# Kernel optimization log

Hardware: AMD Instinct MI355X
Metric: run time of the kernel (lower is better)

## Reference

```python
import jax, jax.numpy as jnp
import numpy as np

DIM = 256
NUM_HEADS = 4
HEAD_DIM = DIM // NUM_HEADS
SCALE = HEAD_DIM ** -0.5


def setup_inputs() -> dict:
    key = jax.random.key(0)
    ks = jax.random.split(key, 11)
    B, Nq, Nkv = 4, 2048, 2048
    inp = {
        "query_feat": jax.random.normal(ks[0], (B, Nq, DIM), dtype=jnp.float32),
        "key_value_feat": jax.random.normal(ks[1], (B, Nkv, DIM), dtype=jnp.float32),
        "reliability_kv": jax.random.uniform(ks[2], (B, Nkv), dtype=jnp.float32),
        "Wq": jax.random.normal(ks[3], (DIM, DIM), dtype=jnp.float32) * (DIM ** -0.5),
        "bq": jnp.zeros((DIM,), jnp.float32),
        "Wk": jax.random.normal(ks[4], (DIM, DIM), dtype=jnp.float32) * (DIM ** -0.5),
        "bk": jnp.zeros((DIM,), jnp.float32),
        "Wv": jax.random.normal(ks[5], (DIM, DIM), dtype=jnp.float32) * (DIM ** -0.5),
        "bv": jnp.zeros((DIM,), jnp.float32),
        "Wo": jax.random.normal(ks[6], (DIM, DIM), dtype=jnp.float32) * (DIM ** -0.5),
        "bo": jnp.zeros((DIM,), jnp.float32),
    }
    return inp


def _heads(x):
    B, N, C = x.shape
    return x.reshape(B, N, NUM_HEADS, HEAD_DIM).transpose(0, 2, 1, 3)  # [B,H,N,hd]


def reference(query_feat, key_value_feat, reliability_kv, Wq, bq, Wk, bk, Wv, bv, Wo, bo):
    B, Nq, _ = query_feat.shape
    q = _heads(query_feat @ Wq + bq)          # [B,H,Nq,hd]
    k = _heads(key_value_feat @ Wk + bk)      # [B,H,Nkv,hd]
    v = _heads(key_value_feat @ Wv + bv)
    # gate K/V by reliability (broadcast over heads and head_dim)
    rk = reliability_kv[:, None, :, None]     # [B,1,Nkv,1]
    k = k * rk
    v = v * rk
    attn = jnp.einsum("bhqd,bhkd->bhqk", q, k) * SCALE
    log_r = jnp.log(jnp.clip(reliability_kv, 1e-6))[:, None, None, :]  # [B,1,1,Nkv]
    attn = jax.nn.softmax(attn + log_r, axis=-1)  # [B,H,Nq,Nkv]
    out = jnp.einsum("bhqk,bhkd->bhqd", attn, v)
    out = out.transpose(0, 2, 1, 3).reshape(B, Nq, DIM)
    out = out @ Wo + bo
    attn_mean = attn.mean(axis=1)  # [B,Nq,Nkv]
    return out, attn_mean
```

## Files before the change

kernel.cpp:

```cpp
#include <hip/hip_runtime.h>


typedef __attribute__((ext_vector_type(8))) _Float16 half8;
typedef __attribute__((ext_vector_type(4))) _Float16 half4;
typedef __attribute__((ext_vector_type(2))) __fp16 fp16x2;
typedef __attribute__((ext_vector_type(4))) float f32x4;

#define MFMAH32(A, B, C) __builtin_amdgcn_mfma_f32_16x16x32_f16((A), (B), (C), 0, 0, 0)
#define MFMAH16(A, B, C) __builtin_amdgcn_mfma_f32_16x16x16f16((A), (B), (C), 0, 0, 0)

__device__ __forceinline__ unsigned short f2h(float f) {
    union { _Float16 h; unsigned short u; } c; c.h = (_Float16)f; return c.u;
}
__device__ __forceinline__ float h2f(unsigned short u) {
    union { unsigned short u; _Float16 h; } c; c.u = u; return (float)c.h;
}
__device__ __forceinline__ half8 ldh8(const unsigned short* p) {
    return *reinterpret_cast<const half8*>(p);
}
__device__ __forceinline__ half4 ldh4(const unsigned short* p) {
    return *reinterpret_cast<const half4*>(p);
}
__device__ __forceinline__ half4 pk4(float a, float b, float c, float d) {
    union { fp16x2 h2[2]; half4 h4; } u;
    u.h2[0] = __builtin_amdgcn_cvt_pkrtz(a, b);
    u.h2[1] = __builtin_amdgcn_cvt_pkrtz(c, d);
    return u.h4;
}
__device__ __forceinline__ void gld16(const unsigned short* g, unsigned short* l) {
    __builtin_amdgcn_global_load_lds(
        (const __attribute__((address_space(1))) unsigned int*)g,
        (__attribute__((address_space(3))) unsigned int*)l, 16, 0, 0);
}

__global__ void wsplit_kernel(const float* __restrict__ Wq, const float* __restrict__ Wk,
                              const float* __restrict__ Wv, const float* __restrict__ Wo,
                              unsigned short* __restrict__ WT) {
    int e = blockIdx.x * 256 + threadIdx.x;
    int m = e >> 16;
    int idx = e & 65535;
    int k = idx >> 8, n = idx & 255;
    const float* W = (m == 0) ? Wq : (m == 1) ? Wk : (m == 2) ? Wv : Wo;
    WT[m * 65536 + n * 256 + k] = f2h(W[idx]);
}

#define STAGE_W(dst_, src_, kt_) do {                                               \
    _Pragma("unroll")                                                               \
    for (int j_ = 0; j_ < 4; ++j_) {                                                \
        int s_ = w * 4 + j_;                                                        \
        int rowl_ = 8 * s_ + (l >> 3);                                              \
        int so_ = rowl_ * 256 + (kt_) * 64 + (((l & 7) ^ (rowl_ & 7)) << 3);        \
        gld16(&(src_)[so_], &(dst_)[s_ * 512]);                                     \
    }                                                                               \
} while (0)

#define GEMM_TILE(buf_, kt_) do {                                                   \
    _Pragma("unroll")                                                               \
    for (int ksl_ = 0; ksl_ < 2; ++ksl_) {                                          \
        _Pragma("unroll")                                                           \
        for (int n_ = 0; n_ < 16; ++n_) {                                           \
            int r_ = n_ * 16 + l15;                                                 \
            int idx_ = r_ * 64 + ((((ksl_)*4 + lg) ^ (r_ & 7)) << 3);               \
            half8 b_ = ldh8(&(buf_)[idx_]);                                         \
            acc[n_] = MFMAH32(ah[(kt_) * 2 + ksl_], b_, acc[n_]);                   \
        }                                                                           \
    }                                                                               \
} while (0)

__global__ __launch_bounds__(512, 1) void proj3_kernel(
    const float* __restrict__ query, const float* __restrict__ kv,
    const float* __restrict__ rel, const unsigned short* __restrict__ WT,
    const float* __restrict__ bq, const float* __restrict__ bk, const float* __restrict__ bv,
    unsigned short* __restrict__ Qh, unsigned short* __restrict__ Kh,
    unsigned short* __restrict__ Vtmp) {
    const int job = blockIdx.y;
    const float* X = (job == 0) ? query : kv;
    const unsigned short* wg = WT + job * 65536;
    const float* bias = (job == 0) ? bq : (job == 1) ? bk : bv;
    const float* rs = (job == 0) ? nullptr : rel;
    unsigned short* oh = (job == 0) ? Qh : (job == 1) ? Kh : Vtmp;

    __shared__ __align__(16) unsigned short wlds[2][256 * 64];

    const int w = threadIdx.x >> 6, l = threadIdx.x & 63;
    const int l15 = l & 15, lg = l >> 4;
    const int arow = blockIdx.x * 128 + w * 16 + l15;

    half8 ah[8];
#pragma unroll
    for (int ks = 0; ks < 8; ++ks) {
        const float* p = &X[arow * 256 + ks * 32 + lg * 8];
        float4 f0 = *reinterpret_cast<const float4*>(p);
        float4 f1 = *reinterpret_cast<const float4*>(p + 4);
        half8 t;
        t[0] = (_Float16)f0.x; t[1] = (_Float16)f0.y; t[2] = (_Float16)f0.z; t[3] = (_Float16)f0.w;
        t[4] = (_Float16)f1.x; t[5] = (_Float16)f1.y; t[6] = (_Float16)f1.z; t[7] = (_Float16)f1.w;
        ah[ks] = t;
    }
    f32x4 acc[16];
#pragma unroll
    for (int n = 0; n < 16; ++n) acc[n] = (f32x4){0.f, 0.f, 0.f, 0.f};

    STAGE_W(wlds[0], wg, 0);
    __syncthreads();
#pragma unroll
    for (int kt = 0; kt < 4; ++kt) {
        const int cur = kt & 1, nx = cur ^ 1;
        if (kt < 3) STAGE_W(wlds[nx], wg, kt + 1);
        GEMM_TILE(wlds[cur], kt);
        __syncthreads();
    }

    const int orow0 = blockIdx.x * 128 + w * 16 + lg * 4;
    float rsv[4];
#pragma unroll
    for (int r = 0; r < 4; ++r) rsv[r] = rs ? rs[orow0 + r] : 1.0f;
#pragma unroll
    for (int n = 0; n < 16; ++n) {
        const int col = n * 16 + l15;
        const float bn = bias[col];
#pragma unroll
        for (int r = 0; r < 4; ++r)
            oh[(orow0 + r) * 256 + col] = f2h((acc[n][r] + bn) * rsv[r]);
    }
}

__global__ void transpose_v_kernel(const unsigned short* __restrict__ Vtmp,
                                   unsigned short* __restrict__ Vt) {
    __shared__ unsigned short tile[16][264];
    const int st = blockIdx.x, b = blockIdx.y;
    const int t = threadIdx.x;
#pragma unroll
    for (int it = 0; it < 4; ++it) {
        int idx = it * 256 + t;
        int kr = idx >> 6;
        int d4 = (idx & 63) * 4;
        ushort4 v = *reinterpret_cast<const ushort4*>(
            &Vtmp[(size_t)(b * 2048 + st * 16 + kr) * 256 + d4]);
        tile[kr][d4 + 0] = v.x; tile[kr][d4 + 1] = v.y;
        tile[kr][d4 + 2] = v.z; tile[kr][d4 + 3] = v.w;
    }
    __syncthreads();
    {
        const int d = t;
        unsigned int u[8];
#pragma unroll
        for (int k2 = 0; k2 < 8; ++k2)
            u[k2] = (unsigned int)tile[k2 * 2][d] | ((unsigned int)tile[k2 * 2 + 1][d] << 16);
        uint4* dst = reinterpret_cast<uint4*>(&Vt[((size_t)(b * 128 + st) * 256 + d) * 16]);
        dst[0] = (uint4){u[0], u[1], u[2], u[3]};
        dst[1] = (uint4){u[4], u[5], u[6], u[7]};
    }
}

__global__ __launch_bounds__(512, 4) void attn_pass1(
    const unsigned short* __restrict__ Qh, const unsigned short* __restrict__ Kh,
    const unsigned short* __restrict__ Vt, const float* __restrict__ rel,
    float* __restrict__ po_a, float* __restrict__ po_b, float* __restrict__ ps) {
    const int bid = blockIdx.x;
    const int sw = (bid & 7) * 64 + (bid >> 3);
    const int b = sw >> 7;
    const int rem = sw & 127;
    const int kh = rem & 1;
    const int q0 = (rem >> 1) * 32;
    const int tid = threadIdx.x;
    const int w = tid >> 6, h = w & 3, ks = w >> 2;
    const int l = tid & 63, l15 = l & 15, lg = l >> 4;
    const float C2 = 0.18033688011112042f;

    __shared__ __align__(16) unsigned short ldsK[8][2][1024];
    __shared__ float rel_lr[2048];
    __shared__ float ssum_sh[2][4][2][16];

    {
        float4 v = reinterpret_cast<const float4*>(&rel[b * 2048])[tid];
        float* d = &rel_lr[tid * 4];
        d[0] = log2f(fmaxf(v.x, 1e-6f)); d[1] = log2f(fmaxf(v.y, 1e-6f));
        d[2] = log2f(fmaxf(v.z, 1e-6f)); d[3] = log2f(fmaxf(v.w, 1e-6f));
    }

    half8 qf[2][2];
#pragma unroll
    for (int qs = 0; qs < 2; ++qs)
#pragma unroll
        for (int kd = 0; kd < 2; ++kd)
            qf[qs][kd] = ldh8(&Qh[(b * 2048 + q0 + qs * 16 + l15) * 256 +
                                  h * 64 + kd * 32 + lg * 8]);
    __syncthreads();

    const int st0 = kh * 64 + ks * 32;

    size_t kb_[2];
    {
        const int swzK = ((l & 7) ^ ((l >> 3) & 7)) << 3;
#pragma unroll
        for (int j = 0; j < 2; ++j) {
            int kr = j * 8 + (l >> 3);
            kb_[j] = (size_t)(b * 2048 + st0 * 16 + kr) * 256 + h * 64 + swzK;
        }
    }
    size_t va_[4];
#pragma unroll
    for (int dc = 0; dc < 4; ++dc)
        va_[dc] = ((size_t)((b * 128 + st0) * 256) + h * 64 + dc * 16 + l15) * 16 + lg * 4;

    unsigned short* myK = &ldsK[w][0][0];
    const int kOff0 = l15 * 64 + ((lg ^ (l15 & 7)) << 3);
    const int kOff1 = l15 * 64 + (((4 + lg) ^ (l15 & 7)) << 3);

#define STGK(buf_, i_) do {                                                         \
    gld16(&Kh[kb_[0] + (size_t)(i_) * 4096], &myK[(buf_) * 1024]);                  \
    gld16(&Kh[kb_[1] + (size_t)(i_) * 4096], &myK[(buf_) * 1024 + 512]);            \
} while (0)
#define VLOADM(dst_, i_) do {                                                       \
    dst_[0] = ldh4(&Vt[va_[0] + (size_t)(i_) * 4096]);                              \
    dst_[1] = ldh4(&Vt[va_[1] + (size_t)(i_) * 4096]);                              \
    dst_[2] = ldh4(&Vt[va_[2] + (size_t)(i_) * 4096]);                              \
    dst_[3] = ldh4(&Vt[va_[3] + (size_t)(i_) * 4096]);                              \
} while (0)

    float ssum0 = 0.f, ssum1 = 0.f;
    f32x4 oacc0[4], oacc1[4];
#pragma unroll
    for (int dc = 0; dc < 4; ++dc) {
        oacc0[dc] = (f32x4){0.f, 0.f, 0.f, 0.f};
        oacc1[dc] = (f32x4){0.f, 0.f, 0.f, 0.f};
    }

#define COMPUTE(step_, BUF_, VF_) do {                                              \
    half8 kf0 = ldh8(&myK[(BUF_) * 1024 + kOff0]);                                  \
    half8 kf1 = ldh8(&myK[(BUF_) * 1024 + kOff1]);                                  \
    f32x4 a0 = (f32x4){0.f, 0.f, 0.f, 0.f}, a1 = a0;                                \
    a0 = MFMAH32(kf0, qf[0][0], a0); a0 = MFMAH32(kf1, qf[0][1], a0);               \
    a1 = MFMAH32(kf0, qf[1][0], a1); a1 = MFMAH32(kf1, qf[1][1], a1);               \
    float4 lr4 = *reinterpret_cast<const float4*>(                                  \
        &rel_lr[(st0 + (step_)) * 16 + lg * 4]);                                    \
    float p00 = exp2f(__builtin_fmaf(a0[0], C2, lr4.x));                            \
    float p01 = exp2f(__builtin_fmaf(a0[1], C2, lr4.y));                            \
    float p02 = exp2f(__builtin_fmaf(a0[2], C2, lr4.z));                            \
    float p03 = exp2f(__builtin_fmaf(a0[3], C2, lr4.w));                            \
    float p10 = exp2f(__builtin_fmaf(a1[0], C2, lr4.x));                            \
    float p11 = exp2f(__builtin_fmaf(a1[1], C2, lr4.y));                            \
    float p12 = exp2f(__builtin_fmaf(a1[2], C2, lr4.z));                            \
    float p13 = exp2f(__builtin_fmaf(a1[3], C2, lr4.w));                            \
    ssum0 += (p00 + p01) + (p02 + p03);                                             \
    ssum1 += (p10 + p11) + (p12 + p13);                                             \
    half4 pa0 = pk4(p00, p01, p02, p03);                                            \
    half4 pa1 = pk4(p10, p11, p12, p13);                                            \
    _Pragma("unroll")                                                               \
    for (int dc = 0; dc < 4; ++dc) {                                                \
        oacc0[dc] = MFMAH16(pa0, VF_[dc], oacc0[dc]);                               \
        oacc1[dc] = MFMAH16(pa1, VF_[dc], oacc1[dc]);                               \
    }                                                                               \
} while (0)

    half4 vfa[4], vfb[4];
    STGK(0, 0);
    VLOADM(vfa, 0);
    for (int i = 0; i < 32; i += 2) {
        STGK(1, i + 1);
        VLOADM(vfb, i + 1);
        asm volatile("s_waitcnt vmcnt(6)" ::: "memory");
        __builtin_amdgcn_sched_barrier(0);
        COMPUTE(i, 0, vfa);
        {
            const int nxt = (i + 2 < 32) ? i + 2 : 31;
            STGK(0, nxt);
            VLOADM(vfa, nxt);
        }
        asm volatile("s_waitcnt vmcnt(6)" ::: "memory");
        __builtin_amdgcn_sched_barrier(0);
        COMPUTE(i + 1, 1, vfb);
    }
    asm volatile("s_waitcnt vmcnt(0)" ::: "memory");
#undef STGK
#undef VLOADM
#undef COMPUTE

    float vr0 = ssum0, vr1 = ssum1;
    vr0 += __shfl_xor(vr0, 16); vr0 += __shfl_xor(vr0, 32);
    vr1 += __shfl_xor(vr1, 16); vr1 += __shfl_xor(vr1, 32);

    __syncthreads();
    if (l < 16) { ssum_sh[ks][h][0][l] = vr0; ssum_sh[ks][h][1][l] = vr1; }
    float* obuf = (float*)&ldsK[0][0][0];
    if (ks == 1) {
#pragma unroll
        for (int qs = 0; qs < 2; ++qs)
#pragma unroll
            for (int dc = 0; dc < 4; ++dc)
#pragma unroll
                for (int r = 0; r < 4; ++r)
                    obuf[(qs * 16 + lg * 4 + r) * 256 + h * 64 + dc * 16 + l15] =
                        (qs == 0) ? oacc0[dc][r] : oacc1[dc][r];
    }
    __syncthreads();
    if (ks == 0) {
        const int chunk = b * 2 + kh;
        float* po = (chunk < 2) ? (po_a + (size_t)chunk * 524288)
                                : (po_b + (size_t)(chunk - 2) * 524288);
#pragma unroll
        for (int qs = 0; qs < 2; ++qs)
#pragma unroll
            for (int dc = 0; dc < 4; ++dc)
#pragma unroll
                for (int r = 0; r < 4; ++r) {
                    const int d = h * 64 + dc * 16 + l15;
                    const int q = qs * 16 + lg * 4 + r;
                    const float mine = (qs == 0) ? oacc0[dc][r] : oacc1[dc][r];
                    po[(size_t)(q0 + q) * 256 + d] = mine + obuf[q * 256 + d];
                }
        if (l < 16) {
            ps[(chunk * 4 + h) * 2048 + q0 + l] =
                ssum_sh[0][h][0][l] + ssum_sh[1][h][0][l];
            ps[(chunk * 4 + h) * 2048 + q0 + 16 + l] =
                ssum_sh[0][h][1][l] + ssum_sh[1][h][1][l];
        }
    }
}

__global__ __launch_bounds__(256) void combine_kernel(
    const float* __restrict__ po_a, const float* __restrict__ po_b,
    const float* __restrict__ ps, unsigned short* __restrict__ AO,
    float* __restrict__ sinv_ws) {
    const int t = blockIdx.x * 256 + threadIdx.x;
    const int d4 = t & 63;
    const int bq = t >> 6;
    const int q = bq & 2047;
    const int b = bq >> 11;
    const int d0 = d4 * 4, h = d0 >> 6;
    const int c0 = b * 2, c1 = b * 2 + 1;
    const float* p0 = (c0 < 2) ? po_a + (size_t)c0 * 524288 : po_b + (size_t)(c0 - 2) * 524288;
    const float* p1 = (c1 < 2) ? po_a + (size_t)c1 * 524288 : po_b + (size_t)(c1 - 2) * 524288;
    float4 x = *reinterpret_cast<const float4*>(&p0[(size_t)q * 256 + d0]);
    float4 y = *reinterpret_cast<const float4*>(&p1[(size_t)q * 256 + d0]);
    float s = ps[(c0 * 4 + h) * 2048 + q] + ps[(c1 * 4 + h) * 2048 + q];
    float si = 1.0f / s;
    ushort4 o;
    o.x = f2h((x.x + y.x) * si); o.y = f2h((x.y + y.y) * si);
    o.z = f2h((x.z + y.z) * si); o.w = f2h((x.w + y.w) * si);
    *reinterpret_cast<ushort4*>(&AO[((size_t)(b * 2048 + q)) * 256 + d0]) = o;
    if (d4 == (h << 4)) sinv_ws[(b * 4 + h) * 2048 + q] = si;
}

__global__ __launch_bounds__(256, 4) void attn_mean_kernel(
    const unsigned short* __restrict__ Qh, const unsigned short* __restrict__ Kh,
    const float* __restrict__ rel, const float* __restrict__ sinv_ws,
    float* __restrict__ attn_mean) {
    const int kslice = blockIdx.x >> 7;
    const int inner = blockIdx.x & 127;
    const int sw = (inner & 7) * 16 + (inner >> 3);
    const int b = sw >> 5;
    const int q0 = (sw & 31) * 64;
    const int tid = threadIdx.x;
    const int w = tid >> 6;
    const int l = tid & 63, l15 = l & 15, lg = l >> 4;
    const int kb = b * 2048;
    const float C2 = 0.18033688011112042f;

    __shared__ __align__(16) unsigned short ldsK[2][8192];
    __shared__ float rel_lr[2048];

    {
        float4 v0 = reinterpret_cast<const float4*>(&rel[b * 2048])[tid * 2];
        float4 v1 = reinterpret_cast<const float4*>(&rel[b * 2048])[tid * 2 + 1];
        float* d = &rel_lr[tid * 8];
        d[0] = log2f(fmaxf(v0.x, 1e-6f)); d[1] = log2f(fmaxf(v0.y, 1e-6f));
        d[2] = log2f(fmaxf(v0.z, 1e-6f)); d[3] = log2f(fmaxf(v0.w, 1e-6f));
        d[4] = log2f(fmaxf(v1.x, 1e-6f)); d[5] = log2f(fmaxf(v1.y, 1e-6f));
        d[6] = log2f(fmaxf(v1.z, 1e-6f)); d[7] = log2f(fmaxf(v1.w, 1e-6f));
    }

    half8 qf[4][2];
    {
        const int qrow = b * 2048 + q0 + w * 16 + l15;
#pragma unroll
        for (int h = 0; h < 4; ++h)
#pragma unroll
            for (int kd = 0; kd < 2; ++kd)
                qf[h][kd] = ldh8(&Qh[qrow * 256 + h * 64 + kd * 32 + lg * 8]);
    }
    float lsi[4][4];
#pragma unroll
    for (int h = 0; h < 4; ++h)
#pragma unroll
        for (int r4 = 0; r4 < 4; ++r4)
            lsi[h][r4] = log2f(sinv_ws[(b * 4 + h) * 2048 + q0 + w * 16 + lg * 4 + r4]) - 2.0f;

    size_t kmb[4];
    {
#pragma unroll
        for (int j = 0; j < 4; ++j) {
            int s_ = w * 4 + j;
            int r_ = 2 * s_ + (l >> 5);
            kmb[j] = (size_t)(kb + r_) * 256 + (((l & 31) ^ (r_ & 7)) << 3);
        }
    }
#define STAGE_KM2(dst_, off_) do {                                                  \
    gld16(&Kh[kmb[0] + (off_)], &(dst_)[(w * 4 + 0) * 512]);                        \
    gld16(&Kh[kmb[1] + (off_)], &(dst_)[(w * 4 + 1) * 512]);                        \
    gld16(&Kh[kmb[2] + (off_)], &(dst_)[(w * 4 + 2) * 512]);                        \
    gld16(&Kh[kmb[3] + (off_)], &(dst_)[(w * 4 + 3) * 512]);                        \
} while (0)

    __syncthreads();

    const int kt0 = kslice * 8;
    size_t moff = (size_t)kt0 * 8192;
    STAGE_KM2(ldsK[0], moff);
    for (int ki = 0; ki < 8; ++ki) {
        const int kt = kt0 + ki;
        const int cur = ki & 1, nx = cur ^ 1;
        if (ki < 7) {
            STAGE_KM2(ldsK[nx], moff + 8192);
            moff += 8192;
            asm volatile("s_waitcnt vmcnt(4)" ::: "memory");
        } else {
            asm volatile("s_waitcnt vmcnt(0)" ::: "memory");
        }
        asm volatile("s_barrier" ::: "memory");
        __builtin_amdgcn_sched_barrier(0);
#pragma unroll
        for (int kc = 0; kc < 2; ++kc) {
            const int r = kc * 16 + l15;
            const int rx = r & 7;
            f32x4 a[4];
#pragma unroll
            for (int h = 0; h < 4; ++h) {
                half8 kf0 = ldh8(&ldsK[cur][r * 256 + (((h * 8 + lg) ^ rx) << 3)]);
                half8 kf1 = ldh8(&ldsK[cur][r * 256 + (((h * 8 + 4 + lg) ^ rx) << 3)]);
                f32x4 t = (f32x4){0.f, 0.f, 0.f, 0.f};
                t = MFMAH32(qf[h][0], kf0, t);
                t = MFMAH32(qf[h][1], kf1, t);
                a[h] = t;
            }
            const float lr = rel_lr[kt * 32 + kc * 16 + l15];
            const size_t kcol = (size_t)(kt * 32 + kc * 16 + l15);
#pragma unroll
            for (int r4 = 0; r4 < 4; ++r4) {
                float m = exp2f(__builtin_fmaf(a[0][r4], C2, lsi[0][r4]) + lr)
                        + exp2f(__builtin_fmaf(a[1][r4], C2, lsi[1][r4]) + lr)
                        + exp2f(__builtin_fmaf(a[2][r4], C2, lsi[2][r4]) + lr)
                        + exp2f(__builtin_fmaf(a[3][r4], C2, lsi[3][r4]) + lr);
                attn_mean[(size_t)(b * 2048 + q0 + w * 16 + lg * 4 + r4) * 2048 + kcol] = m;
            }
        }
        asm volatile("s_waitcnt lgkmcnt(0)\n\ts_barrier" ::: "memory");
    }
#undef STAGE_KM2
}

__global__ __launch_bounds__(512, 1) void final_kernel(
    const unsigned short* __restrict__ AO, const unsigned short* __restrict__ WoT,
    const float* __restrict__ bo, float* __restrict__ out) {
    __shared__ __align__(16) unsigned short wlds[2][256 * 64];

    const int w = threadIdx.x >> 6, l = threadIdx.x & 63;
    const int l15 = l & 15, lg = l >> 4;
    const int arow = blockIdx.x * 128 + w * 16 + l15;

    half8 ah[8];
#pragma unroll
    for (int ks = 0; ks < 8; ++ks)
        ah[ks] = ldh8(&AO[arow * 256 + ks * 32 + lg * 8]);
    f32x4 acc[16];
#pragma unroll
    for (int n = 0; n < 16; ++n) acc[n] = (f32x4){0.f, 0.f, 0.f, 0.f};

    STAGE_W(wlds[0], WoT, 0);
    __syncthreads();
#pragma unroll
    for (int kt = 0; kt < 4; ++kt) {
        const int cur = kt & 1, nx = cur ^ 1;
        if (kt < 3) STAGE_W(wlds[nx], WoT, kt + 1);
        GEMM_TILE(wlds[cur], kt);
        __syncthreads();
    }

    const int orow0 = blockIdx.x * 128 + w * 16 + lg * 4;
#pragma unroll
    for (int n = 0; n < 16; ++n) {
        const int col = n * 16 + l15;
        const float bn = bo[col];
#pragma unroll
        for (int r = 0; r < 4; ++r)
            out[(orow0 + r) * 256 + col] = acc[n][r] + bn;
    }
}

extern "C" void kernel_launch(void* const* d_in, const int* in_sizes, int n_in,
                              void* d_out, int out_size, void* d_ws, size_t ws_size,
                              hipStream_t stream) {
    const float* query = (const float*)d_in[0];
    const float* kv    = (const float*)d_in[1];
    const float* rel   = (const float*)d_in[2];
    const float* Wq    = (const float*)d_in[3];
    const float* bq    = (const float*)d_in[4];
    const float* Wk    = (const float*)d_in[5];
    const float* bk    = (const float*)d_in[6];
    const float* Wv    = (const float*)d_in[7];
    const float* bv    = (const float*)d_in[8];
    const float* Wo    = (const float*)d_in[9];
    const float* bo    = (const float*)d_in[10];

    char* ws = (char*)d_ws;
    unsigned short* WT   = (unsigned short*)(ws + 0);
    unsigned short* Qh   = (unsigned short*)(ws + 524288);
    unsigned short* Kh   = (unsigned short*)(ws + 4718592);
    unsigned short* Vtmp = (unsigned short*)(ws + 8912896);
    unsigned short* Vt   = (unsigned short*)(ws + 13107200);
    unsigned short* AO   = (unsigned short*)(ws + 17301504);
    float*          sinv = (float*)(ws + 21495808);
    float*          ps   = (float*)(ws + 21626880);
    float*          po_b = (float*)(ws + 21889024);
    float*          po_a = (float*)Vtmp;

    float* out = (float*)d_out;
    float* attn_mean = (float*)d_out + 2097152;

    wsplit_kernel<<<1024, 256, 0, stream>>>(Wq, Wk, Wv, Wo, WT);
    proj3_kernel<<<dim3(64, 3), 512, 0, stream>>>(query, kv, rel, WT,
                                                  bq, bk, bv, Qh, Kh, Vtmp);
    transpose_v_kernel<<<dim3(128, 4), 256, 0, stream>>>(Vtmp, Vt);
    attn_pass1<<<512, 512, 0, stream>>>(Qh, Kh, Vt, rel, po_a, po_b, ps);
    combine_kernel<<<2048, 256, 0, stream>>>(po_a, po_b, ps, AO, sinv);
    attn_mean_kernel<<<1024, 256, 0, stream>>>(Qh, Kh, rel, sinv, attn_mean);
    final_kernel<<<64, 512, 0, stream>>>(AO, WT + 3 * 65536, bo, out);
}
```

Baseline: 105.0 us.

## Fuse split-K combine into final GEMM and deepen attn K/V pipeline to four stages

After: 134.4 us. +28.1%, slower.

```diff
diff --git a/kernel.cpp b/kernel.cpp
--- a/kernel.cpp
+++ b/kernel.cpp
@@ -168,7 +168,7 @@
     const int l = tid & 63, l15 = l & 15, lg = l >> 4;
     const float C2 = 0.18033688011112042f;
 
-    __shared__ __align__(16) unsigned short ldsK[8][2][1024];
+    __shared__ __align__(16) unsigned short ldsK[8][4][1024];
     __shared__ float rel_lr[2048];
     __shared__ float ssum_sh[2][4][2][16];
 
@@ -208,9 +208,9 @@
     const int kOff0 = l15 * 64 + ((lg ^ (l15 & 7)) << 3);
     const int kOff1 = l15 * 64 + (((4 + lg) ^ (l15 & 7)) << 3);
 
-#define STGK(buf_, i_) do {                                                         \
-    gld16(&Kh[kb_[0] + (size_t)(i_) * 4096], &myK[(buf_) * 1024]);                  \
-    gld16(&Kh[kb_[1] + (size_t)(i_) * 4096], &myK[(buf_) * 1024 + 512]);            \
+#define STGK(slot_, i_) do {                                                        \
+    gld16(&Kh[kb_[0] + (size_t)(i_) * 4096], &myK[(slot_) * 1024]);                 \
+    gld16(&Kh[kb_[1] + (size_t)(i_) * 4096], &myK[(slot_) * 1024 + 512]);           \
 } while (0)
 #define VLOADM(dst_, i_) do {                                                       \
     dst_[0] = ldh4(&Vt[va_[0] + (size_t)(i_) * 4096]);                              \
@@ -227,9 +227,9 @@
         oacc1[dc] = (f32x4){0.f, 0.f, 0.f, 0.f};
     }
 
-#define COMPUTE(step_, BUF_, VF_) do {                                              \
-    half8 kf0 = ldh8(&myK[(BUF_) * 1024 + kOff0]);                                  \
-    half8 kf1 = ldh8(&myK[(BUF_) * 1024 + kOff1]);                                  \
+#define COMPUTE(step_, SLOT_, VF_) do {                                             \
+    half8 kf0 = ldh8(&myK[(SLOT_) * 1024 + kOff0]);                                 \
+    half8 kf1 = ldh8(&myK[(SLOT_) * 1024 + kOff1]);                                 \
     f32x4 a0 = (f32x4){0.f, 0.f, 0.f, 0.f}, a1 = a0;                                \
     a0 = MFMAH32(kf0, qf[0][0], a0); a0 = MFMAH32(kf1, qf[0][1], a0);               \
     a1 = MFMAH32(kf0, qf[1][0], a1); a1 = MFMAH32(kf1, qf[1][1], a1);               \
@@ -254,23 +254,30 @@
     }                                                                               \
 } while (0)
 
-    half4 vfa[4], vfb[4];
-    STGK(0, 0);
-    VLOADM(vfa, 0);
-    for (int i = 0; i < 32; i += 2) {
-        STGK(1, i + 1);
-        VLOADM(vfb, i + 1);
-        asm volatile("s_waitcnt vmcnt(6)" ::: "memory");
+    half4 vf0[4], vf1[4], vf2[4], vf3[4];
+    STGK(0, 0); VLOADM(vf0, 0);
+    STGK(1, 1); VLOADM(vf1, 1);
+    for (int i = 0; i < 32; i += 4) {
+        {   int nxt = (i + 2 < 32) ? i + 2 : 31;
+            STGK(2, nxt); VLOADM(vf2, nxt); }
+        asm volatile("s_waitcnt vmcnt(12)" ::: "memory");
         __builtin_amdgcn_sched_barrier(0);
-        COMPUTE(i, 0, vfa);
-        {
-            const int nxt = (i + 2 < 32) ? i + 2 : 31;
-            STGK(0, nxt);
-            VLOADM(vfa, nxt);
-        }
-        asm volatile("s_waitcnt vmcnt(6)" ::: "memory");
+        COMPUTE(i, 0, vf0);
+        {   int nxt = (i + 3 < 32) ? i + 3 : 31;
+            STGK(3, nxt); VLOADM(vf3, nxt); }
+        asm volatile("s_waitcnt vmcnt(12)" ::: "memory");
         __builtin_amdgcn_sched_barrier(0);
-        COMPUTE(i + 1, 1, vfb);
+        COMPUTE(i + 1, 1, vf1);
+        {   int nxt = (i + 4 < 32) ? i + 4 : 31;
+            STGK(0, nxt); VLOADM(vf0, nxt); }
+        asm volatile("s_waitcnt vmcnt(12)" ::: "memory");
+        __builtin_amdgcn_sched_barrier(0);
+        COMPUTE(i + 2, 2, vf2);
+        {   int nxt = (i + 5 < 32) ? i + 5 : 31;
+            STGK(1, nxt); VLOADM(vf1, nxt); }
+        asm volatile("s_waitcnt vmcnt(12)" ::: "memory");
+        __builtin_amdgcn_sched_barrier(0);
+        COMPUTE(i + 3, 3, vf3);
     }
     asm volatile("s_waitcnt vmcnt(0)" ::: "memory");
 #undef STGK
@@ -319,33 +326,9 @@
     }
 }
 
-__global__ __launch_bounds__(256) void combine_kernel(
-    const float* __restrict__ po_a, const float* __restrict__ po_b,
-    const float* __restrict__ ps, unsigned short* __restrict__ AO,
-    float* __restrict__ sinv_ws) {
-    const int t = blockIdx.x * 256 + threadIdx.x;
-    const int d4 = t & 63;
-    const int bq = t >> 6;
-    const int q = bq & 2047;
-    const int b = bq >> 11;
-    const int d0 = d4 * 4, h = d0 >> 6;
-    const int c0 = b * 2, c1 = b * 2 + 1;
-    const float* p0 = (c0 < 2) ? po_a + (size_t)c0 * 524288 : po_b + (size_t)(c0 - 2) * 524288;
-    const float* p1 = (c1 < 2) ? po_a + (size_t)c1 * 524288 : po_b + (size_t)(c1 - 2) * 524288;
-    float4 x = *reinterpret_cast<const float4*>(&p0[(size_t)q * 256 + d0]);
-    float4 y = *reinterpret_cast<const float4*>(&p1[(size_t)q * 256 + d0]);
-    float s = ps[(c0 * 4 + h) * 2048 + q] + ps[(c1 * 4 + h) * 2048 + q];
-    float si = 1.0f / s;
-    ushort4 o;
-    o.x = f2h((x.x + y.x) * si); o.y = f2h((x.y + y.y) * si);
-    o.z = f2h((x.z + y.z) * si); o.w = f2h((x.w + y.w) * si);
-    *reinterpret_cast<ushort4*>(&AO[((size_t)(b * 2048 + q)) * 256 + d0]) = o;
-    if (d4 == (h << 4)) sinv_ws[(b * 4 + h) * 2048 + q] = si;
-}
-
 __global__ __launch_bounds__(256, 4) void attn_mean_kernel(
     const unsigned short* __restrict__ Qh, const unsigned short* __restrict__ Kh,
-    const float* __restrict__ rel, const float* __restrict__ sinv_ws,
+    const float* __restrict__ rel, const float* __restrict__ ps,
     float* __restrict__ attn_mean) {
     const int kslice = blockIdx.x >> 7;
     const int inner = blockIdx.x & 127;
@@ -384,8 +367,12 @@
 #pragma unroll
     for (int h = 0; h < 4; ++h)
 #pragma unroll
-        for (int r4 = 0; r4 < 4; ++r4)
-            lsi[h][r4] = log2f(sinv_ws[(b * 4 + h) * 2048 + q0 + w * 16 + lg * 4 + r4]) - 2.0f;
+        for (int r4 = 0; r4 < 4; ++r4) {
+            const int qq = q0 + w * 16 + lg * 4 + r4;
+            float s = ps[((2 * b) * 4 + h) * 2048 + qq] +
+                      ps[((2 * b + 1) * 4 + h) * 2048 + qq];
+            lsi[h][r4] = -log2f(s) - 2.0f;
+        }
 
     size_t kmb[4];
     {
@@ -451,18 +438,40 @@
 }
 
 __global__ __launch_bounds__(512, 1) void final_kernel(
-    const unsigned short* __restrict__ AO, const unsigned short* __restrict__ WoT,
+    const float* __restrict__ po_a, const float* __restrict__ po_b,
+    const float* __restrict__ ps, const unsigned short* __restrict__ WoT,
     const float* __restrict__ bo, float* __restrict__ out) {
     __shared__ __align__(16) unsigned short wlds[2][256 * 64];
 
     const int w = threadIdx.x >> 6, l = threadIdx.x & 63;
     const int l15 = l & 15, lg = l >> 4;
     const int arow = blockIdx.x * 128 + w * 16 + l15;
+    const int bb = arow >> 11, qq = arow & 2047;
+    const int c0 = bb * 2, c1 = c0 + 1;
+    const float* p0 = (c0 < 2) ? po_a + (size_t)c0 * 524288 : po_b + (size_t)(c0 - 2) * 524288;
+    const float* p1 = (c1 < 2) ? po_a + (size_t)c1 * 524288 : po_b + (size_t)(c1 - 2) * 524288;
+
+    float si[4];
+#pragma unroll
+    for (int h = 0; h < 4; ++h)
+        si[h] = 1.0f / (ps[(c0 * 4 + h) * 2048 + qq] + ps[(c1 * 4 + h) * 2048 + qq]);
 
     half8 ah[8];
 #pragma unroll
-    for (int ks = 0; ks < 8; ++ks)
-        ah[ks] = ldh8(&AO[arow * 256 + ks * 32 + lg * 8]);
+    for (int ks = 0; ks < 8; ++ks) {
+        const int d0 = ks * 32 + lg * 8;
+        float4 x0 = *reinterpret_cast<const float4*>(&p0[(size_t)qq * 256 + d0]);
+        float4 x1 = *reinterpret_cast<const float4*>(&p0[(size_t)qq * 256 + d0 + 4]);
+        float4 y0 = *reinterpret_cast<const float4*>(&p1[(size_t)qq * 256 + d0]);
+        float4 y1 = *reinterpret_cast<const float4*>(&p1[(size_t)qq * 256 + d0 + 4]);
+        const float s_ = si[ks >> 1];
+        half8 t;
+        t[0] = (_Float16)((x0.x + y0.x) * s_); t[1] = (_Float16)((x0.y + y0.y) * s_);
+        t[2] = (_Float16)((x0.z + y0.z) * s_); t[3] = (_Float16)((x0.w + y0.w) * s_);
+        t[4] = (_Float16)((x1.x + y1.x) * s_); t[5] = (_Float16)((x1.y + y1.y) * s_);
+        t[6] = (_Float16)((x1.z + y1.z) * s_); t[7] = (_Float16)((x1.w + y1.w) * s_);
+        ah[ks] = t;
+    }
     f32x4 acc[16];
 #pragma unroll
     for (int n = 0; n < 16; ++n) acc[n] = (f32x4){0.f, 0.f, 0.f, 0.f};
@@ -509,8 +518,6 @@
     unsigned short* Kh   = (unsigned short*)(ws + 4718592);
     unsigned short* Vtmp = (unsigned short*)(ws + 8912896);
     unsigned short* Vt   = (unsigned short*)(ws + 13107200);
-    unsigned short* AO   = (unsigned short*)(ws + 17301504);
-    float*          sinv = (float*)(ws + 21495808);
     float*          ps   = (float*)(ws + 21626880);
     float*          po_b = (float*)(ws + 21889024);
     float*          po_a = (float*)Vtmp;
@@ -523,7 +530,6 @@
                                                   bq, bk, bv, Qh, Kh, Vtmp);
     transpose_v_kernel<<<dim3(128, 4), 256, 0, stream>>>(Vtmp, Vt);
     attn_pass1<<<512, 512, 0, stream>>>(Qh, Kh, Vt, rel, po_a, po_b, ps);
-    combine_kernel<<<2048, 256, 0, stream>>>(po_a, po_b, ps, AO, sinv);
-    attn_mean_kernel<<<1024, 256, 0, stream>>>(Qh, Kh, rel, sinv, attn_mean);
-    final_kernel<<<64, 512, 0, stream>>>(AO, WT + 3 * 65536, bo, out);
-}
+    attn_mean_kernel<<<1024, 256, 0, stream>>>(Qh, Kh, rel, ps, attn_mean);
+    final_kernel<<<64, 512, 0, stream>>>(po_a, po_b, ps, WT + 3 * 65536, bo, out);
+}
```

## Deepen attention K prefetch to four LDS slots and split final GEMM finer

Applied to the files above, without the earlier changes.

New measurement: 107.7 us. 1.03x slower.

```diff
diff --git a/kernel.cpp b/kernel.cpp
--- a/kernel.cpp
+++ b/kernel.cpp
@@ -48,6 +48,16 @@
     _Pragma("unroll")                                                               \
     for (int j_ = 0; j_ < 4; ++j_) {                                                \
         int s_ = w * 4 + j_;                                                        \
+        int rowl_ = 8 * s_ + (l >> 3);                                              \
+        int so_ = rowl_ * 256 + (kt_) * 64 + (((l & 7) ^ (rowl_ & 7)) << 3);        \
+        gld16(&(src_)[so_], &(dst_)[s_ * 512]);                                     \
+    }                                                                               \
+} while (0)
+
+#define STAGE_W8(dst_, src_, kt_) do {                                              \
+    _Pragma("unroll")                                                               \
+    for (int j_ = 0; j_ < 8; ++j_) {                                                \
+        int s_ = w * 8 + j_;                                                        \
         int rowl_ = 8 * s_ + (l >> 3);                                              \
         int so_ = rowl_ * 256 + (kt_) * 64 + (((l & 7) ^ (rowl_ & 7)) << 3);        \
         gld16(&(src_)[so_], &(dst_)[s_ * 512]);                                     \
@@ -168,7 +178,7 @@
     const int l = tid & 63, l15 = l & 15, lg = l >> 4;
     const float C2 = 0.18033688011112042f;
 
-    __shared__ __align__(16) unsigned short ldsK[8][2][1024];
+    __shared__ __align__(16) unsigned short ldsK[8][4][1024];
     __shared__ float rel_lr[2048];
     __shared__ float ssum_sh[2][4][2][16];
 
@@ -208,9 +218,9 @@
     const int kOff0 = l15 * 64 + ((lg ^ (l15 & 7)) << 3);
     const int kOff1 = l15 * 64 + (((4 + lg) ^ (l15 & 7)) << 3);
 
-#define STGK(buf_, i_) do {                                                         \
-    gld16(&Kh[kb_[0] + (size_t)(i_) * 4096], &myK[(buf_) * 1024]);                  \
-    gld16(&Kh[kb_[1] + (size_t)(i_) * 4096], &myK[(buf_) * 1024 + 512]);            \
+#define STGK(slot_, i_) do {                                                        \
+    gld16(&Kh[kb_[0] + (size_t)(i_) * 4096], &myK[(slot_) * 1024]);                 \
+    gld16(&Kh[kb_[1] + (size_t)(i_) * 4096], &myK[(slot_) * 1024 + 512]);           \
 } while (0)
 #define VLOADM(dst_, i_) do {                                                       \
     dst_[0] = ldh4(&Vt[va_[0] + (size_t)(i_) * 4096]);                              \
@@ -227,9 +237,9 @@
         oacc1[dc] = (f32x4){0.f, 0.f, 0.f, 0.f};
     }
 
-#define COMPUTE(step_, BUF_, VF_) do {                                              \
-    half8 kf0 = ldh8(&myK[(BUF_) * 1024 + kOff0]);                                  \
-    half8 kf1 = ldh8(&myK[(BUF_) * 1024 + kOff1]);                                  \
+#define COMPUTE(step_, SLOT_, VF_) do {                                             \
+    half8 kf0 = ldh8(&myK[(SLOT_) * 1024 + kOff0]);                                 \
+    half8 kf1 = ldh8(&myK[(SLOT_) * 1024 + kOff1]);                                 \
     f32x4 a0 = (f32x4){0.f, 0.f, 0.f, 0.f}, a1 = a0;                                \
     a0 = MFMAH32(kf0, qf[0][0], a0); a0 = MFMAH32(kf1, qf[0][1], a0);               \
     a1 = MFMAH32(kf0, qf[1][0], a1); a1 = MFMAH32(kf1, qf[1][1], a1);               \
@@ -255,22 +265,30 @@
 } while (0)
 
     half4 vfa[4], vfb[4];
+    VLOADM(vfa, 0);
     STGK(0, 0);
-    VLOADM(vfa, 0);
-    for (int i = 0; i < 32; i += 2) {
-        STGK(1, i + 1);
-        VLOADM(vfb, i + 1);
-        asm volatile("s_waitcnt vmcnt(6)" ::: "memory");
+    STGK(1, 1);
+    for (int i = 0; i < 32; i += 4) {
+        {   int nxt = (i + 2 < 32) ? i + 2 : 31;
+            STGK(2, nxt); VLOADM(vfb, (i + 1 < 32) ? i + 1 : 31); }
+        asm volatile("s_waitcnt vmcnt(8)" ::: "memory");
         __builtin_amdgcn_sched_barrier(0);
         COMPUTE(i, 0, vfa);
-        {
-            const int nxt = (i + 2 < 32) ? i + 2 : 31;
-            STGK(0, nxt);
-            VLOADM(vfa, nxt);
-        }
-        asm volatile("s_waitcnt vmcnt(6)" ::: "memory");
+        {   int nxt = (i + 3 < 32) ? i + 3 : 31;
+            STGK(3, nxt); VLOADM(vfa, (i + 2 < 32) ? i + 2 : 31); }
+        asm volatile("s_waitcnt vmcnt(8)" ::: "memory");
         __builtin_amdgcn_sched_barrier(0);
         COMPUTE(i + 1, 1, vfb);
+        {   int nxt = (i + 4 < 32) ? i + 4 : 31;
+            STGK(0, nxt); VLOADM(vfb, (i + 3 < 32) ? i + 3 : 31); }
+        asm volatile("s_waitcnt vmcnt(8)" ::: "memory");
+        __builtin_amdgcn_sched_barrier(0);
+        COMPUTE(i + 2, 2, vfa);
+        {   int nxt = (i + 5 < 32) ? i + 5 : 31;
+            STGK(1, nxt); VLOADM(vfa, (i + 4 < 32) ? i + 4 : 31); }
+        asm volatile("s_waitcnt vmcnt(8)" ::: "memory");
+        __builtin_amdgcn_sched_barrier(0);
+        COMPUTE(i + 3, 3, vfb);
     }
     asm volatile("s_waitcnt vmcnt(0)" ::: "memory");
 #undef STGK
@@ -450,14 +468,14 @@
 #undef STAGE_KM2
 }
 
-__global__ __launch_bounds__(512, 1) void final_kernel(
+__global__ __launch_bounds__(256, 2) void final_kernel(
     const unsigned short* __restrict__ AO, const unsigned short* __restrict__ WoT,
     const float* __restrict__ bo, float* __restrict__ out) {
     __shared__ __align__(16) unsigned short wlds[2][256 * 64];
 
     const int w = threadIdx.x >> 6, l = threadIdx.x & 63;
     const int l15 = l & 15, lg = l >> 4;
-    const int arow = blockIdx.x * 128 + w * 16 + l15;
+    const int arow = blockIdx.x * 64 + w * 16 + l15;
 
     half8 ah[8];
 #pragma unroll
@@ -467,17 +485,17 @@
 #pragma unroll
     for (int n = 0; n < 16; ++n) acc[n] = (f32x4){0.f, 0.f, 0.f, 0.f};
 
-    STAGE_W(wlds[0], WoT, 0);
+    STAGE_W8(wlds[0], WoT, 0);
     __syncthreads();
 #pragma unroll
     for (int kt = 0; kt < 4; ++kt) {
         const int cur = kt & 1, nx = cur ^ 1;
-        if (kt < 3) STAGE_W(wlds[nx], WoT, kt + 1);
+        if (kt < 3) STAGE_W8(wlds[nx], WoT, kt + 1);
         GEMM_TILE(wlds[cur], kt);
         __syncthreads();
     }
 
-    const int orow0 = blockIdx.x * 128 + w * 16 + lg * 4;
+    const int orow0 = blockIdx.x * 64 + w * 16 + lg * 4;
 #pragma unroll
     for (int n = 0; n < 16; ++n) {
         const int col = n * 16 + l15;
@@ -525,5 +543,5 @@
     attn_pass1<<<512, 512, 0, stream>>>(Qh, Kh, Vt, rel, po_a, po_b, ps);
     combine_kernel<<<2048, 256, 0, stream>>>(po_a, po_b, ps, AO, sinv);
     attn_mean_kernel<<<1024, 256, 0, stream>>>(Qh, Kh, rel, sinv, attn_mean);
-    final_kernel<<<64, 512, 0, stream>>>(AO, WT + 3 * 65536, bo, out);
-}
+    final_kernel<<<128, 256, 0, stream>>>(AO, WT + 3 * 65536, bo, out);
+}
```
